# Kernel optimization log

Hardware: AMD Instinct MI355X
Metric: run time of the kernel (lower is better)

## Reference

```python
import jax, jax.numpy as jnp
import numpy as np

B, N, D_FEAT = 16, 4096, 64
NPOINT, NSAMPLE = 1024, 32
MLP = [64, 64, 128]
IN_CH = 3 + D_FEAT
EPS = 1e-5  # BatchNorm eps (torch default)


def _fps(xyz, npoint):
    # Farthest point sampling; sequential scan over npoint steps (matches torch loop).
    b, n, _ = xyz.shape
    def step(carry, _):
        distance, farthest = carry  # (B,N) running min dist, (B,) current centroid idx
        centroid = jnp.take_along_axis(xyz, farthest[:, None, None], axis=1)  # (B,1,3)
        d = jnp.sum((xyz - centroid) ** 2, -1)  # (B,N)
        distance = jnp.minimum(distance, d)
        nxt = jnp.argmax(distance, -1).astype(jnp.int32)
        return (distance, nxt), farthest
    init = (jnp.full((b, n), jnp.inf, dtype=xyz.dtype),
            jnp.full((b,), n // 2, dtype=jnp.int32))
    _, centroids = jax.lax.scan(step, init, None, length=npoint)
    return centroids.T  # (B, npoint)


def _gather(pts, idx):
    # pts: (B,N,C); idx: (B,...) int -> (B,...,C)
    return jax.vmap(lambda p, i: p[i])(pts, idx)


def setup_inputs() -> dict:
    key = jax.random.key(0)
    ks = jax.random.split(key, 16)
    inp = {
        'xyz': jax.random.normal(ks[0], (B, N, 3), jnp.float32),
        'points': jax.random.normal(ks[1], (B, N, D_FEAT), jnp.float32),
    }
    last = IN_CH
    for li, oc in enumerate(MLP):
        inp[f'W{li}'] = jax.random.normal(ks[2 + li], (oc, last), jnp.float32) * (1.0 / np.sqrt(last))
        inp[f'b{li}'] = jnp.zeros((oc,), jnp.float32)
        inp[f'g{li}'] = jnp.ones((oc,), jnp.float32)
        inp[f'be{li}'] = jnp.zeros((oc,), jnp.float32)
        last = oc
    C = MLP[-1]; R = C // 8
    inp['aW1'] = jax.random.normal(ks[10], (R, C), jnp.float32) * (1.0 / np.sqrt(C))
    inp['aW2'] = jax.random.normal(ks[11], (C, R), jnp.float32) * (1.0 / np.sqrt(R))
    return inp


def reference(xyz, points, W0, b0, g0, be0, W1, b1, g1, be1, W2, b2, g2, be2, aW1, aW2):
    fps_idx = _fps(xyz, NPOINT)                 # (B,S) int32
    new_xyz = _gather(xyz, fps_idx)             # (B,S,3)
    # squared distances (B,S,N) via matmul expansion (as torch square_distance)
    d = (-2.0 * jnp.einsum('bsc,bnc->bsn', new_xyz, xyz)
         + jnp.sum(new_xyz ** 2, -1)[..., None]
         + jnp.sum(xyz ** 2, -1)[:, None, :])
    _, idx = jax.lax.top_k(-d, NSAMPLE)         # (B,S,k) nearest neighbors
    grouped_xyz = _gather(xyz, idx)             # (B,S,k,3)
    rel = grouped_xyz - new_xyz[:, :, None, :]  # relative coords
    feat = _gather(points, idx)                 # (B,S,k,D)
    g = jnp.concatenate([rel, feat], axis=-1)   # (B,S,k,3+D) channels-last
    # 1x1 conv MLP + BatchNorm (training-mode batch stats) + ReLU
    for (W, b, ga, be) in ((W0, b0, g0, be0), (W1, b1, g1, be1), (W2, b2, g2, be2)):
        g = jnp.einsum('bskc,oc->bsko', g, W) + b
        mu = g.mean(axis=(0, 1, 2))
        var = g.var(axis=(0, 1, 2))
        g = ga * (g - mu) * jax.lax.rsqrt(var + EPS) + be
        g = jax.nn.relu(g)
    new_points = g.max(axis=2)                  # max over nsample -> (B,S,C)
    # channel attention on (B,C,S) == reductions over S here
    avg = new_points.mean(axis=1)               # (B,C)
    mx = new_points.max(axis=1)                 # (B,C)
    def fc(v):
        return jnp.einsum('cr,br->bc', aW2, jax.nn.relu(jnp.einsum('rc,bc->br', aW1, v)))
    scale = jax.nn.sigmoid(fc(avg) + fc(mx))    # (B,C)
    new_points = new_points * scale[:, None, :]
    return new_xyz, new_points, fps_idx
```

## Files before the change

kernel.cpp:

```cpp
#include <hip/hip_runtime.h>
#include <hip/hip_bf16.h>

#define BB 16
#define NN 4096
#define SS 1024
#define KS 32
#define DF 64
#define INC 67
#define C1 64
#define C2 64
#define C3 128
#define ROWS (BB*SS*KS)
#define EPSBN 1e-5f
#define F_INF (__builtin_inff())

typedef __bf16 bf16;
typedef __bf16 bfrag __attribute__((ext_vector_type(8)));
typedef float  ffrag __attribute__((ext_vector_type(4)));
typedef float  f2    __attribute__((ext_vector_type(2)));
typedef unsigned long long u64;

#define OUT_NXYZ 0
#define OUT_NP   49152
#define OUT_FPS  2146304

#define OFF_FPS   0u
#define OFF_NXYZ  65536u
#define OFF_IDX   262144u
#define OFF_STATS 2359296u
#define OFF_ASUM  2555904u
#define OFF_AMAX  2621440u
#define OFF_BNC   2686976u
#define OFF_SCALE 2690048u
#define OFF_NP0   2698240u
#define OFF_YMAX  11086848u
#define OFF_H1    19475456u
#define OFF_H2    86584320u
#define ZERO_BYTES (196608u + 65536u + 65536u)

#define DPP_MAX_STEP(k, ctrl, rmask, bc) { \
  int _lo = __builtin_amdgcn_update_dpp(0, (int)(unsigned)(k), (ctrl), (rmask), 0xf, (bc)); \
  int _hi = __builtin_amdgcn_update_dpp(0, (int)((k)>>32),     (ctrl), (rmask), 0xf, (bc)); \
  u64 _k2 = ((u64)(unsigned)_hi << 32) | (unsigned)_lo; \
  if (_k2 > (k)) (k) = _k2; }

#define DPP_FMAX_STEP(v, ctrl, rmask) { \
  int _s = __builtin_amdgcn_update_dpp(0, __float_as_int(v), (ctrl), (rmask), 0xf, true); \
  v = fmaxf(v, __int_as_float(_s)); }

#define DPP_UMAX_STEP(v, ctrl, rmask) { \
  unsigned _s = (unsigned)__builtin_amdgcn_update_dpp(0, (int)(v), (ctrl), (rmask), 0xf, true); \
  if (_s > (v)) (v) = _s; }

__device__ __forceinline__ float dpp_wavemax_f32(float v){
  DPP_FMAX_STEP(v, 0x111, 0xf) DPP_FMAX_STEP(v, 0x112, 0xf)
  DPP_FMAX_STEP(v, 0x114, 0xf) DPP_FMAX_STEP(v, 0x118, 0xf)
  DPP_FMAX_STEP(v, 0x142, 0xa) DPP_FMAX_STEP(v, 0x143, 0xc)
  return v;
}
__device__ __forceinline__ unsigned dpp_wavemax_u32(unsigned v){
  DPP_UMAX_STEP(v, 0x111, 0xf) DPP_UMAX_STEP(v, 0x112, 0xf)
  DPP_UMAX_STEP(v, 0x114, 0xf) DPP_UMAX_STEP(v, 0x118, 0xf)
  DPP_UMAX_STEP(v, 0x142, 0xa) DPP_UMAX_STEP(v, 0x143, 0xc)
  return v;
}
__device__ __forceinline__ u64 dpp_wavemax64(u64 k){
  DPP_MAX_STEP(k, 0x111, 0xf, true)
  DPP_MAX_STEP(k, 0x112, 0xf, true)
  DPP_MAX_STEP(k, 0x114, 0xf, true)
  DPP_MAX_STEP(k, 0x118, 0xf, true)
  DPP_MAX_STEP(k, 0x142, 0xa, false)
  DPP_MAX_STEP(k, 0x143, 0xc, false)
  return k;
}
__device__ __forceinline__ u64 bcast63(u64 k){
  unsigned lo = (unsigned)__builtin_amdgcn_readlane((int)(unsigned)k, 63);
  unsigned hi = (unsigned)__builtin_amdgcn_readlane((int)(k>>32), 63);
  return ((u64)hi<<32) | lo;
}

__global__ __launch_bounds__(256) void fps_kernel(const float* __restrict__ xyz,
                                                  int* __restrict__ fps_i,
                                                  float* __restrict__ nxyz_ws,
                                                  float* __restrict__ out)
{
  #pragma clang fp contract(off)
  __shared__ float lx[NN], ly[NN], lz[NN];
  __shared__ int lfps[SS];
  __shared__ u64 slotk[2][4];
  int b = blockIdx.x, t = threadIdx.x;
  const float* xb = xyz + (size_t)b*NN*3;
  for (int p = t; p < NN; p += 256){ lx[p]=xb[p*3]; ly[p]=xb[p*3+1]; lz[p]=xb[p*3+2]; }
  __syncthreads();
  f2 px2[8], py2[8], pz2[8], pd2[8];
  int p0 = t*16;
  #pragma unroll
  for (int j=0;j<8;++j){
    px2[j] = (f2){lx[p0+2*j], lx[p0+2*j+1]};
    py2[j] = (f2){ly[p0+2*j], ly[p0+2*j+1]};
    pz2[j] = (f2){lz[p0+2*j], lz[p0+2*j+1]};
    pd2[j] = (f2){F_INF, F_INF};
  }
  float cx = lx[NN/2], cy = ly[NN/2], cz = lz[NN/2];
  if (t==0) lfps[0]=NN/2;
  int wv = t >> 6, lane = t & 63;
  for (int it=1; it<SS; ++it){
    f2 c2x = (f2){cx,cx}, c2y = (f2){cy,cy}, c2z = (f2){cz,cz};
    f2 ma = (f2){-1.f,-1.f}, mb = (f2){-1.f,-1.f};
    #pragma unroll
    for (int j=0;j<8;++j){
      f2 dx = px2[j]-c2x, dy = py2[j]-c2y, dz = pz2[j]-c2z;
      f2 d = (dx*dx + dy*dy) + dz*dz;
      f2 nd = (f2){fminf(pd2[j].x, d.x), fminf(pd2[j].y, d.y)};
      pd2[j]=nd;
      if (j & 1){ mb = (f2){fmaxf(mb.x, nd.x), fmaxf(mb.y, nd.y)}; }
      else      { ma = (f2){fmaxf(ma.x, nd.x), fmaxf(ma.y, nd.y)}; }
    }
    float wm = fmaxf(fmaxf(ma.x, ma.y), fmaxf(mb.x, mb.y));
    float gv = dpp_wavemax_f32(wm);
    gv = __int_as_float(__builtin_amdgcn_readlane(__float_as_int(gv), 63));
    unsigned cand = 0xFFFFFFFFu;
    #pragma unroll
    for (int j=7;j>=0;--j){
      if (pd2[j].y == gv) cand = (unsigned)(p0+2*j+1);
      if (pd2[j].x == gv) cand = (unsigned)(p0+2*j);
    }
    unsigned nidx = dpp_wavemax_u32(~cand);
    int p = it & 1;
    if (lane == 63) slotk[p][wv] = ((u64)__float_as_uint(gv) << 32) | nidx;
    __syncthreads();
    u64 k = slotk[p][t & 3];
    DPP_MAX_STEP(k, 0xB1, 0xf, true)
    DPP_MAX_STEP(k, 0x4E, 0xf, true)
    int i = ~(unsigned)k;
    cx = lx[i]; cy = ly[i]; cz = lz[i];
    if (t==0) lfps[it]=i;
  }
  __syncthreads();
  for (int s=t; s<SS; s+=256){
    int i = lfps[s];
    fps_i[b*SS+s]=i;
    out[OUT_FPS + b*SS + s] = (float)i;
    float xx=lx[i], yy=ly[i], zz=lz[i];
    int o3 = (b*SS+s)*3;
    out[OUT_NXYZ+o3]=xx; out[OUT_NXYZ+o3+1]=yy; out[OUT_NXYZ+o3+2]=zz;
    nxyz_ws[o3]=xx; nxyz_ws[o3+1]=yy; nxyz_ws[o3+2]=zz;
  }
}

__global__ __launch_bounds__(64) void knn_kernel(const float* __restrict__ xyz,
                                                 const float* __restrict__ nxyz,
                                                 int* __restrict__ knn)
{
  __shared__ float ld[NN];
  int lane = threadIdx.x;
  int bs = blockIdx.x;
  int b = bs >> 10;
  const float* xb = xyz + (size_t)b*NN*3;
  float sx=nxyz[bs*3], sy=nxyz[bs*3+1], sz=nxyz[bs*3+2];
  float gv[8]; int gi[8];
  float lv = F_INF; int li = 0;
  #pragma unroll
  for (int g=0; g<8; ++g){
    float bgv = F_INF; int bgi = 0;
    #pragma unroll
    for (int jj=0; jj<8; ++jj){
      int p = (g*8+jj)*64 + lane;
      float dx=xb[p*3]-sx, dy=xb[p*3+1]-sy, dz=xb[p*3+2]-sz;
      float d = dx*dx+dy*dy+dz*dz;
      ld[p] = d;
      if (d < bgv){ bgv=d; bgi=p; }
    }
    gv[g]=bgv; gi[g]=bgi;
    if (bgv < lv){ lv=bgv; li=bgi; }
  }
  int kept = 0;
  for (int it=0; it<KS; ++it){
    u64 mk = ~(((u64)__float_as_uint(lv) << 32) | (unsigned)li);
    mk = dpp_wavemax64(mk);
    mk = bcast63(mk);
    int i = (int)(unsigned)(~mk);
    if (lane==it) kept = i;
    if ((i & 63) == lane){
      int j = i >> 6;
      ld[i] = F_INF;
      int g = j >> 3;
      float bgv=F_INF; int bgi=0;
      for (int jj=0;jj<8;++jj){
        int p = (g*8+jj)*64 + lane;
        float d = ld[p];
        if (d<bgv){bgv=d;bgi=p;}
      }
      #pragma unroll
      for (int q=0;q<8;++q){ if (q==g){ gv[q]=bgv; gi[q]=bgi; } }
      lv=F_INF; li=0;
      #pragma unroll
      for (int q=0;q<8;++q){ if (gv[q]<lv){ lv=gv[q]; li=gi[q]; } }
    }
  }
  if (lane < KS) knn[bs*KS + lane] = kept;
}

__global__ __launch_bounds__(256) void conv1_kernel(const float* __restrict__ xyz,
                                                    const float* __restrict__ points,
                                                    const float* __restrict__ W0,
                                                    const float* __restrict__ b0,
                                                    const float* __restrict__ nxyz,
                                                    const int* __restrict__ knn,
                                                    bf16* __restrict__ h1,
                                                    float* __restrict__ stats)
{
  __shared__ __align__(16) bf16 As[64][104];
  __shared__ __align__(16) bf16 Bs[64][104];
  __shared__ float s1[C1], s2[C1];
  int t = threadIdx.x;
  int Rbase = blockIdx.x * 64;
  if (t < C1){ s1[t]=0.f; s2[t]=0.f; }
  {
    int o = t >> 2, q = t & 3;
    const float* wr = W0 + o*INC;
    for (int cc = q*24; cc < q*24+24; ++cc){
      float w;
      if (cc < 64) w = wr[3+cc];
      else if (cc < 67) w = wr[cc-64];
      else w = 0.f;
      Bs[o][cc] = (bf16)w;
    }
  }
  {
    int r = t >> 2, q = t & 3;
    int R = Rbase + r;
    int bs = R >> 5;
    int bIdx = bs >> 10;
    int nI = knn[R];
    const float* pr = points + ((size_t)(bIdx*NN + nI))*DF + q*16;
    float4 f0 = *(const float4*)(pr);
    float4 f1 = *(const float4*)(pr+4);
    float4 f2v = *(const float4*)(pr+8);
    float4 f3 = *(const float4*)(pr+12);
    bf16* ap = &As[r][q*16];
    ap[0]=(bf16)f0.x; ap[1]=(bf16)f0.y; ap[2]=(bf16)f0.z; ap[3]=(bf16)f0.w;
    ap[4]=(bf16)f1.x; ap[5]=(bf16)f1.y; ap[6]=(bf16)f1.z; ap[7]=(bf16)f1.w;
    ap[8]=(bf16)f2v.x; ap[9]=(bf16)f2v.y; ap[10]=(bf16)f2v.z; ap[11]=(bf16)f2v.w;
    ap[12]=(bf16)f3.x; ap[13]=(bf16)f3.y; ap[14]=(bf16)f3.z; ap[15]=(bf16)f3.w;
    if (q==0){
      const float* xr = xyz + ((size_t)(bIdx*NN + nI))*3;
      const float* nr = nxyz + bs*3;
      As[r][64]=(bf16)(xr[0]-nr[0]);
      As[r][65]=(bf16)(xr[1]-nr[1]);
      As[r][66]=(bf16)(xr[2]-nr[2]);
      for (int cc=67; cc<96; ++cc) As[r][cc]=(bf16)0.f;
    }
  }
  __syncthreads();
  int wv = t >> 6, lane = t & 63;
  int row16 = wv * 16;
  int arow = lane & 15, kgrp = lane >> 4;
  ffrag acc[4] = {};
  #pragma unroll
  for (int kc = 0; kc < 3; ++kc){
    bfrag af = *(const bfrag*)&As[row16 + arow][kc*32 + kgrp*8];
    #pragma unroll
    for (int nt = 0; nt < 4; ++nt){
      bfrag bfv = *(const bfrag*)&Bs[nt*16 + arow][kc*32 + kgrp*8];
      acc[nt] = __builtin_amdgcn_mfma_f32_16x16x32_bf16(af, bfv, acc[nt], 0,0,0);
    }
  }
  #pragma unroll
  for (int nt=0; nt<4; ++nt){
    int c = nt*16 + arow;
    float bias = b0[c];
    float ls1=0.f, ls2=0.f;
    #pragma unroll
    for (int r=0;r<4;++r){
      float y = acc[nt][r] + bias;
      int grow = Rbase + row16 + kgrp*4 + r;
      h1[(size_t)grow*C1 + c] = (bf16)y;
      ls1 += y; ls2 += y*y;
    }
    ls1 += __shfl_xor(ls1, 16); ls1 += __shfl_xor(ls1, 32);
    ls2 += __shfl_xor(ls2, 16); ls2 += __shfl_xor(ls2, 32);
    if (kgrp==0){ atomicAdd(&s1[c], ls1); atomicAdd(&s2[c], ls2); }
  }
  __syncthreads();
  if (t < C1){
    float* gp = stats + (blockIdx.x & 63)*256;
    atomicAdd(&gp[t], s1[t]);
    atomicAdd(&gp[128 + t], s2[t]);
  }
}

__global__ void bnfin_kernel(const float* __restrict__ stats, const float* __restrict__ g,
                             const float* __restrict__ be, float* __restrict__ bnc, int C)
{
  int c = threadIdx.x; if (c >= C) return;
  float a1=0.f, a2=0.f;
  for (int q=0;q<64;++q){ a1 += stats[q*256+c]; a2 += stats[q*256+128+c]; }
  float inv = 1.f/(float)ROWS;
  float mu = a1*inv; float var = a2*inv - mu*mu;
  float a = g[c]*rsqrtf(var + EPSBN);
  bnc[c] = a; bnc[128+c] = be[c] - mu*a;
}

__global__ __launch_bounds__(256) void conv2_kernel(const bf16* __restrict__ h1,
                                                    const float* __restrict__ W1,
                                                    const float* __restrict__ b1,
                                                    const float* __restrict__ bnc,
                                                    bf16* __restrict__ h2,
                                                    float* __restrict__ stats)
{
  __shared__ __align__(16) bf16 As[64][72];
  __shared__ __align__(16) bf16 Bs[64][72];
  __shared__ float s1[C2], s2[C2];
  int t = threadIdx.x;
  int Rbase = blockIdx.x * 64;
  if (t < C2){ s1[t]=0.f; s2[t]=0.f; }
  {
    int o = t >> 2, q = t & 3;
    const float* wr = W1 + o*64 + q*16;
    bf16* bp = &Bs[o][q*16];
    #pragma unroll
    for (int v=0; v<4; ++v){
      float4 f = *(const float4*)(wr + v*4);
      bp[v*4+0]=(bf16)f.x; bp[v*4+1]=(bf16)f.y; bp[v*4+2]=(bf16)f.z; bp[v*4+3]=(bf16)f.w;
    }
  }
  {
    int r = t >> 2, q = t & 3;
    int R = Rbase + r;
    const bf16* hr = h1 + (size_t)R*64 + q*16;
    bfrag h0 = *(const bfrag*)hr;
    bfrag h1v = *(const bfrag*)(hr+8);
    #pragma unroll
    for (int j=0;j<8;++j){
      int c=q*16+j;
      As[r][c] = (bf16)fmaxf(fmaf(bnc[c], (float)h0[j], bnc[128+c]), 0.f);
    }
    #pragma unroll
    for (int j=0;j<8;++j){
      int c=q*16+8+j;
      As[r][c] = (bf16)fmaxf(fmaf(bnc[c], (float)h1v[j], bnc[128+c]), 0.f);
    }
  }
  __syncthreads();
  int wv = t >> 6, lane = t & 63;
  int row16 = wv * 16;
  int arow = lane & 15, kgrp = lane >> 4;
  ffrag acc[4] = {};
  #pragma unroll
  for (int kc = 0; kc < 2; ++kc){
    bfrag af = *(const bfrag*)&As[row16 + arow][kc*32 + kgrp*8];
    #pragma unroll
    for (int nt = 0; nt < 4; ++nt){
      bfrag bfv = *(const bfrag*)&Bs[nt*16 + arow][kc*32 + kgrp*8];
      acc[nt] = __builtin_amdgcn_mfma_f32_16x16x32_bf16(af, bfv, acc[nt], 0,0,0);
    }
  }
  #pragma unroll
  for (int nt=0; nt<4; ++nt){
    int c = nt*16 + arow;
    float bias = b1[c];
    float ls1=0.f, ls2=0.f;
    #pragma unroll
    for (int r=0;r<4;++r){
      float y = acc[nt][r] + bias;
      int grow = Rbase + row16 + kgrp*4 + r;
      h2[(size_t)grow*C2 + c] = (bf16)y;
      ls1 += y; ls2 += y*y;
    }
    ls1 += __shfl_xor(ls1, 16); ls1 += __shfl_xor(ls1, 32);
    ls2 += __shfl_xor(ls2, 16); ls2 += __shfl_xor(ls2, 32);
    if (kgrp==0){ atomicAdd(&s1[c], ls1); atomicAdd(&s2[c], ls2); }
  }
  __syncthreads();
  if (t < C2){
    float* gp = stats + (blockIdx.x & 63)*256;
    atomicAdd(&gp[t], s1[t]);
    atomicAdd(&gp[128 + t], s2[t]);
  }
}

__global__ __launch_bounds__(256) void conv3_kernel(const bf16* __restrict__ h2,
                                                    const float* __restrict__ W2,
                                                    const float* __restrict__ b2,
                                                    const float* __restrict__ bnc,
                                                    float* __restrict__ ymax,
                                                    float* __restrict__ stats)
{
  __shared__ __align__(16) bf16 As[64][72];
  __shared__ __align__(16) bf16 Bs[128][72];
  __shared__ float s1[C3], s2[C3];
  __shared__ float wmax[4][C3];
  int t = threadIdx.x;
  int Rbase = blockIdx.x * 64;
  if (t < C3){ s1[t]=0.f; s2[t]=0.f; }
  {
    int o = t >> 1, q = t & 1;
    const float* wr = W2 + o*64 + q*32;
    bf16* bp = &Bs[o][q*32];
    #pragma unroll
    for (int v=0; v<8; ++v){
      float4 f = *(const float4*)(wr + v*4);
      bp[v*4+0]=(bf16)f.x; bp[v*4+1]=(bf16)f.y; bp[v*4+2]=(bf16)f.z; bp[v*4+3]=(bf16)f.w;
    }
  }
  {
    int r = t >> 2, q = t & 3;
    int R = Rbase + r;
    const bf16* hr = h2 + (size_t)R*64 + q*16;
    bfrag h0 = *(const bfrag*)hr;
    bfrag h1v = *(const bfrag*)(hr+8);
    #pragma unroll
    for (int j=0;j<8;++j){
      int c=q*16+j;
      As[r][c] = (bf16)fmaxf(fmaf(bnc[c], (float)h0[j], bnc[128+c]), 0.f);
    }
    #pragma unroll
    for (int j=0;j<8;++j){
      int c=q*16+8+j;
      As[r][c] = (bf16)fmaxf(fmaf(bnc[c], (float)h1v[j], bnc[128+c]), 0.f);
    }
  }
  __syncthreads();
  int wv = t >> 6, lane = t & 63;
  int row16 = wv * 16;
  int arow = lane & 15, kgrp = lane >> 4;
  ffrag acc[8] = {};
  #pragma unroll
  for (int kc = 0; kc < 2; ++kc){
    bfrag af = *(const bfrag*)&As[row16 + arow][kc*32 + kgrp*8];
    #pragma unroll
    for (int nt = 0; nt < 8; ++nt){
      bfrag bfv = *(const bfrag*)&Bs[nt*16 + arow][kc*32 + kgrp*8];
      acc[nt] = __builtin_amdgcn_mfma_f32_16x16x32_bf16(af, bfv, acc[nt], 0,0,0);
    }
  }
  #pragma unroll
  for (int nt=0; nt<8; ++nt){
    int c = nt*16 + arow;
    float bias = b2[c];
    float ls1=0.f, ls2=0.f, mm=-F_INF;
    #pragma unroll
    for (int r=0;r<4;++r){
      float y = acc[nt][r] + bias;
      ls1 += y; ls2 += y*y; mm = fmaxf(mm, y);
    }
    ls1 += __shfl_xor(ls1, 16); ls1 += __shfl_xor(ls1, 32);
    ls2 += __shfl_xor(ls2, 16); ls2 += __shfl_xor(ls2, 32);
    mm = fmaxf(mm, __shfl_xor(mm, 16)); mm = fmaxf(mm, __shfl_xor(mm, 32));
    if (kgrp==0){ atomicAdd(&s1[c], ls1); atomicAdd(&s2[c], ls2); wmax[wv][c]=mm; }
  }
  __syncthreads();
  {
    int half = t >> 7;
    int c = t & 127;
    float m = fmaxf(wmax[half*2][c], wmax[half*2+1][c]);
    ymax[(size_t)(blockIdx.x*2 + half)*C3 + c] = m;
  }
  if (t < C3){
    float* gp = stats + (blockIdx.x & 63)*256;
    atomicAdd(&gp[t], s1[t]);
    atomicAdd(&gp[128 + t], s2[t]);
  }
}

__global__ __launch_bounds__(256) void attreduce_kernel(const float* __restrict__ ymax,
                                                        const float* __restrict__ bnc,
                                                        float* __restrict__ np0,
                                                        float* __restrict__ asum,
                                                        unsigned* __restrict__ amax)
{
  __shared__ float rs[256], rm[256];
  int t = threadIdx.x;
  int b = blockIdx.x >> 3, sg = blockIdx.x & 7;
  int c = t & 127, h = t >> 7;
  float a = bnc[c], bb = bnc[128+c];
  size_t base = ((size_t)(b*1024 + sg*128 + h*64))*128 + c;
  float s = 0.f, m = 0.f;
  #pragma unroll 4
  for (int j=0;j<64;++j){
    float v = fmaxf(fmaf(a, ymax[base + (size_t)j*128], bb), 0.f);
    np0[base + (size_t)j*128] = v;
    s += v; m = fmaxf(m, v);
  }
  rs[t]=s; rm[t]=m;
  __syncthreads();
  if (t < 128){
    float s2 = rs[t] + rs[t+128];
    float m2 = fmaxf(rm[t], rm[t+128]);
    atomicAdd(&asum[b*128+t], s2);
    atomicMax(&amax[b*128+t], __float_as_uint(m2));
  }
}

__global__ __launch_bounds__(256) void attn_kernel(const float* __restrict__ asum,
                                                   const unsigned* __restrict__ amax,
                                                   const float* __restrict__ aW1,
                                                   const float* __restrict__ aW2,
                                                   float* __restrict__ scale)
{
  __shared__ float avg[16][128], mx[16][128], hA[16][16], hM[16][16];
  int t = threadIdx.x;
  for (int i=t; i<2048; i+=256){
    int b=i>>7, c=i&127;
    avg[b][c]=asum[i]*(1.f/1024.f); mx[b][c]=__uint_as_float(amax[i]);
  }
  __syncthreads();
  {
    int b=t>>4, r=t&15;
    float sa=0.f, sm=0.f;
    for (int c=0;c<128;++c){ float w=aW1[r*128+c]; sa+=w*avg[b][c]; sm+=w*mx[b][c]; }
    hA[b][r]=fmaxf(sa,0.f); hM[b][r]=fmaxf(sm,0.f);
  }
  __syncthreads();
  for (int i=t;i<2048;i+=256){
    int b=i>>7,c=i&127;
    float o=0.f;
    for (int r=0;r<16;++r){ o += aW2[c*16+r]*(hA[b][r]+hM[b][r]); }
    scale[i] = 1.f/(1.f+expf(-o));
  }
}

__global__ __launch_bounds__(256) void finout_kernel(const float* __restrict__ np0,
                                                     const float* __restrict__ scale,
                                                     float* __restrict__ out)
{
  int i = blockIdx.x*256 + threadIdx.x;
  int c = i & 127; int b = i >> 17;
  out[OUT_NP + i] = np0[i] * scale[b*128+c];
}

extern "C" void kernel_launch(void* const* d_in, const int* in_sizes, int n_in,
                              void* d_out, int out_size, void* d_ws, size_t ws_size,
                              hipStream_t stream)
{
  const float* xyz    = (const float*)d_in[0];
  const float* points = (const float*)d_in[1];
  const float* W0 = (const float*)d_in[2];
  const float* b0 = (const float*)d_in[3];
  const float* g0 = (const float*)d_in[4];
  const float* be0= (const float*)d_in[5];
  const float* W1 = (const float*)d_in[6];
  const float* b1 = (const float*)d_in[7];
  const float* g1 = (const float*)d_in[8];
  const float* be1= (const float*)d_in[9];
  const float* W2 = (const float*)d_in[10];
  const float* b2 = (const float*)d_in[11];
  const float* g2 = (const float*)d_in[12];
  const float* be2= (const float*)d_in[13];
  const float* aW1= (const float*)d_in[14];
  const float* aW2= (const float*)d_in[15];
  float* out = (float*)d_out;
  char* ws = (char*)d_ws;

  int*      fpsI  = (int*)(ws + OFF_FPS);
  float*    nxyz  = (float*)(ws + OFF_NXYZ);
  int*      knnI  = (int*)(ws + OFF_IDX);
  float*    stats = (float*)(ws + OFF_STATS);
  float*    asum  = (float*)(ws + OFF_ASUM);
  unsigned* amax  = (unsigned*)(ws + OFF_AMAX);
  float*    bnc   = (float*)(ws + OFF_BNC);
  float*    scl   = (float*)(ws + OFF_SCALE);
  float*    np0   = (float*)(ws + OFF_NP0);
  float*    ymax  = (float*)(ws + OFF_YMAX);
  bf16*     h1    = (bf16*)(ws + OFF_H1);
  bf16*     h2    = (bf16*)(ws + OFF_H2);

  hipMemsetAsync(ws + OFF_STATS, 0, ZERO_BYTES, stream);
  fps_kernel<<<BB, 256, 0, stream>>>(xyz, fpsI, nxyz, out);
  knn_kernel<<<BB*SS, 64, 0, stream>>>(xyz, nxyz, knnI);
  conv1_kernel<<<ROWS/64, 256, 0, stream>>>(xyz, points, W0, b0, nxyz, knnI, h1, stats);
  bnfin_kernel<<<1, 128, 0, stream>>>(stats, g0, be0, bnc, C1);
  conv2_kernel<<<ROWS/64, 256, 0, stream>>>(h1, W1, b1, bnc, h2, stats + 64*256);
  bnfin_kernel<<<1, 128, 0, stream>>>(stats + 64*256, g1, be1, bnc + 256, C2);
  conv3_kernel<<<ROWS/64, 256, 0, stream>>>(h2, W2, b2, bnc + 256, ymax, stats + 2*64*256);
  bnfin_kernel<<<1, 128, 0, stream>>>(stats + 2*64*256, g2, be2, bnc + 512, C3);
  attreduce_kernel<<<BB*8, 256, 0, stream>>>(ymax, bnc + 512, np0, asum, amax);
  attn_kernel<<<1, 256, 0, stream>>>(asum, amax, aW1, aW2, scl);
  finout_kernel<<<(BB*SS*C3)/256, 256, 0, stream>>>(np0, scl, out);
}
```

Before: 1.112 ms.

## Pack two FPS batches per 512-thread block in fps_kernel

FPS now processes two batch elements per workgroup, with 512 threads split into two 256-thread groups that share one block barrier per iteration. The launch drops to 8 blocks, so fewer CUs are used, and each block's shared memory doubles. Both groups must step in lockstep, so each barrier waits on both batches. The likely motive is to change CU and SIMD scheduling of this latency-bound sequential loop, but it could slow things if the two groups contend for the same CU's SIMDs.

After: 1.390 ms. 24.9% more time.

```diff
diff --git a/kernel.cpp b/kernel.cpp
--- a/kernel.cpp
+++ b/kernel.cpp
@@ -79,31 +79,34 @@
   return ((u64)hi<<32) | lo;
 }
 
-__global__ __launch_bounds__(256) void fps_kernel(const float* __restrict__ xyz,
+__global__ __launch_bounds__(512) void fps_kernel(const float* __restrict__ xyz,
                                                   int* __restrict__ fps_i,
                                                   float* __restrict__ nxyz_ws,
                                                   float* __restrict__ out)
 {
   #pragma clang fp contract(off)
-  __shared__ float lx[NN], ly[NN], lz[NN];
-  __shared__ int lfps[SS];
-  __shared__ u64 slotk[2][4];
-  int b = blockIdx.x, t = threadIdx.x;
+  __shared__ float lx[2][NN], ly[2][NN], lz[2][NN];
+  __shared__ int lfps[2][SS];
+  __shared__ u64 slotk[2][2][4];
+  int t = threadIdx.x;
+  int g = t >> 8;
+  int tt = t & 255;
+  int b = blockIdx.x*2 + g;
   const float* xb = xyz + (size_t)b*NN*3;
-  for (int p = t; p < NN; p += 256){ lx[p]=xb[p*3]; ly[p]=xb[p*3+1]; lz[p]=xb[p*3+2]; }
+  for (int p = tt; p < NN; p += 256){ lx[g][p]=xb[p*3]; ly[g][p]=xb[p*3+1]; lz[g][p]=xb[p*3+2]; }
   __syncthreads();
   f2 px2[8], py2[8], pz2[8], pd2[8];
-  int p0 = t*16;
+  int p0 = tt*16;
   #pragma unroll
   for (int j=0;j<8;++j){
-    px2[j] = (f2){lx[p0+2*j], lx[p0+2*j+1]};
-    py2[j] = (f2){ly[p0+2*j], ly[p0+2*j+1]};
-    pz2[j] = (f2){lz[p0+2*j], lz[p0+2*j+1]};
+    px2[j] = (f2){lx[g][p0+2*j], lx[g][p0+2*j+1]};
+    py2[j] = (f2){ly[g][p0+2*j], ly[g][p0+2*j+1]};
+    pz2[j] = (f2){lz[g][p0+2*j], lz[g][p0+2*j+1]};
     pd2[j] = (f2){F_INF, F_INF};
   }
-  float cx = lx[NN/2], cy = ly[NN/2], cz = lz[NN/2];
-  if (t==0) lfps[0]=NN/2;
-  int wv = t >> 6, lane = t & 63;
+  float cx = lx[g][NN/2], cy = ly[g][NN/2], cz = lz[g][NN/2];
+  if (tt==0) lfps[g][0]=NN/2;
+  int wv = tt >> 6, lane = t & 63;
   for (int it=1; it<SS; ++it){
     f2 c2x = (f2){cx,cx}, c2y = (f2){cy,cy}, c2z = (f2){cz,cz};
     f2 ma = (f2){-1.f,-1.f}, mb = (f2){-1.f,-1.f};
@@ -127,21 +130,21 @@
     }
     unsigned nidx = dpp_wavemax_u32(~cand);
     int p = it & 1;
-    if (lane == 63) slotk[p][wv] = ((u64)__float_as_uint(gv) << 32) | nidx;
+    if (lane == 63) slotk[p][g][wv] = ((u64)__float_as_uint(gv) << 32) | nidx;
     __syncthreads();
-    u64 k = slotk[p][t & 3];
+    u64 k = slotk[p][g][t & 3];
     DPP_MAX_STEP(k, 0xB1, 0xf, true)
     DPP_MAX_STEP(k, 0x4E, 0xf, true)
     int i = ~(unsigned)k;
-    cx = lx[i]; cy = ly[i]; cz = lz[i];
-    if (t==0) lfps[it]=i;
-  }
-  __syncthreads();
-  for (int s=t; s<SS; s+=256){
-    int i = lfps[s];
+    cx = lx[g][i]; cy = ly[g][i]; cz = lz[g][i];
+    if (tt==0) lfps[g][it]=i;
+  }
+  __syncthreads();
+  for (int s=tt; s<SS; s+=256){
+    int i = lfps[g][s];
     fps_i[b*SS+s]=i;
     out[OUT_FPS + b*SS + s] = (float)i;
-    float xx=lx[i], yy=ly[i], zz=lz[i];
+    float xx=lx[g][i], yy=ly[g][i], zz=lz[g][i];
     int o3 = (b*SS+s)*3;
     out[OUT_NXYZ+o3]=xx; out[OUT_NXYZ+o3+1]=yy; out[OUT_NXYZ+o3+2]=zz;
     nxyz_ws[o3]=xx; nxyz_ws[o3+1]=yy; nxyz_ws[o3+2]=zz;
@@ -567,7 +570,7 @@
   bf16*     h2    = (bf16*)(ws + OFF_H2);
 
   hipMemsetAsync(ws + OFF_STATS, 0, ZERO_BYTES, stream);
-  fps_kernel<<<BB, 256, 0, stream>>>(xyz, fpsI, nxyz, out);
+  fps_kernel<<<BB/2, 512, 0, stream>>>(xyz, fpsI, nxyz, out);
   knn_kernel<<<BB*SS, 64, 0, stream>>>(xyz, nxyz, knnI);
   conv1_kernel<<<ROWS/64, 256, 0, stream>>>(xyz, points, W0, b0, nxyz, knnI, h1, stats);
   bnfin_kernel<<<1, 128, 0, stream>>>(stats, g0, be0, bnc, C1);
```
